# Kernel tuning notes

Hardware: AMD Instinct MI355X
Metric: run time of the kernel (lower is better)

## Reference

```python
import jax, jax.numpy as jnp
import numpy as np

N2, S2, M2 = 20000, 16000, 4000   # hop-2 frontier, hop-2 src fanout, hop-2 dst nodes
S1, M1 = 3500, 1024               # hop-1 src fanout, final batch
D_IN, D_H = 128, 128              # input_dim, internal_dim


def setup_inputs() -> dict:
    key = jax.random.key(0)
    ks = jax.random.split(key, 9)
    return {
        "src_nodes": jax.random.normal(ks[0], (N2, D_IN), dtype=jnp.float32),
        "dstsrc2src_1": jax.random.randint(ks[1], (S1,), 0, M2, dtype=jnp.int64),
        "dstsrc2src_2": jax.random.randint(ks[2], (S2,), 0, N2, dtype=jnp.int64),
        "dstsrc2dst_1": jax.random.randint(ks[3], (M1,), 0, M2, dtype=jnp.int64),
        "dstsrc2dst_2": jax.random.randint(ks[4], (M2,), 0, N2, dtype=jnp.int64),
        "dif_mat_1": jax.random.uniform(ks[5], (M1, S1), dtype=jnp.float32),
        "dif_mat_2": jax.random.uniform(ks[6], (M2, S2), dtype=jnp.float32),
        "w1": jax.random.normal(ks[7], (2 * D_IN, D_H), dtype=jnp.float32) * 0.06,
        "w2": jax.random.normal(ks[8], (2 * D_H, D_H), dtype=jnp.float32) * 0.06,
    }


def _mean_aggregate(feats, dstsrc2src, dstsrc2dst, dif_mat, w):
    # gather -> diffusion matmul -> concat -> linear -> relu
    dst_features = feats[dstsrc2dst]               # [M, d]
    src_features = feats[dstsrc2src]               # [S, d]
    aggregated = dif_mat @ src_features            # [M, d]
    concatenated = jnp.concatenate([aggregated, dst_features], axis=1)  # [M, 2d]
    return jax.nn.relu(concatenated @ w)           # [M, d_out]


def reference(src_nodes, dstsrc2src_1, dstsrc2src_2, dstsrc2dst_1,
              dstsrc2dst_2, dif_mat_1, dif_mat_2, w1, w2):
    # GraphSage.call: hop-2 aggregator first (with *_2 inputs), then hop-1.
    x = _mean_aggregate(src_nodes, dstsrc2src_2, dstsrc2dst_2, dif_mat_2, w1)
    x = _mean_aggregate(x, dstsrc2src_1, dstsrc2dst_1, dif_mat_1, w2)
    return x
```

## Files before the change

kernel.cpp:

```cpp
#include <hip/hip_runtime.h>

typedef __bf16 bf16x8 __attribute__((ext_vector_type(8)));
typedef float  f32x4  __attribute__((ext_vector_type(4)));
typedef unsigned short u16;
typedef u16 u16x8 __attribute__((ext_vector_type(8)));

__device__ __forceinline__ u16 f2bf(float f) {
    unsigned u = __builtin_bit_cast(unsigned, f);
    return (u16)((u + 0x7FFFu + ((u >> 16) & 1u)) >> 16);
}

__global__ __launch_bounds__(256) void gather_bt(
    const float* __restrict__ feats, const int* __restrict__ idx,
    u16* __restrict__ Bt, int Kcnt, int Kpad)
{
    __shared__ u16 st[128][66];
    const int tid = threadIdx.x;
    const int k0  = blockIdx.x * 64;

#pragma unroll
    for (int r2 = 0; r2 < 64; r2 += 2) {
        int r = r2 + (tid >> 7);
        int c = tid & 127;
        int k = k0 + r;
        float v = 0.f;
        if (k < Kcnt) v = feats[(size_t)idx[k] * 128 + c];
        st[c][r] = f2bf(v);
    }
    __syncthreads();

#pragma unroll
    for (int p = 0; p < 4; ++p) {
        int n  = p * 32 + (tid >> 3);
        int kk = (tid & 7) * 8;
        u16x8 v;
#pragma unroll
        for (int j = 0; j < 8; ++j) v[j] = st[n][kk + j];
        *(u16x8*)(Bt + (size_t)n * Kpad + k0 + kk) = v;
    }
}

__device__ __forceinline__ void loadA8(const float* __restrict__ ap, int koff,
                                       int K, f32x4& a0, f32x4& a1)
{
    if (koff + 8 <= K) {
        a0 = *(const f32x4*)(ap + koff);
        a1 = *(const f32x4*)(ap + koff + 4);
    } else {
#pragma unroll
        for (int j = 0; j < 4; ++j) {
            a0[j] = (koff + j     < K) ? ap[koff + j]     : 0.f;
            a1[j] = (koff + 4 + j < K) ? ap[koff + 4 + j] : 0.f;
        }
    }
}

__device__ __forceinline__ bf16x8 packA(f32x4 a0, f32x4 a1) {
    u16x8 h;
    h[0]=f2bf(a0[0]); h[1]=f2bf(a0[1]); h[2]=f2bf(a0[2]); h[3]=f2bf(a0[3]);
    h[4]=f2bf(a1[0]); h[5]=f2bf(a1[1]); h[6]=f2bf(a1[2]); h[7]=f2bf(a1[3]);
    return __builtin_bit_cast(bf16x8, h);
}

__global__ __launch_bounds__(256) void gemm_bt(
    const float* __restrict__ A, const u16* __restrict__ Bt,
    float* __restrict__ C, int M, int K, int Kpad, int sps)
{
    const int wid  = threadIdx.x >> 6;
    const int lane = threadIdx.x & 63;
    const int l15  = lane & 15;
    const int lhi  = lane >> 4;

    const int row0  = blockIdx.x * 64 + wid * 16;
    const int total = (K + 31) >> 5;
    int s0 = blockIdx.y * sps;
    int s1 = s0 + sps; if (s1 > total) s1 = total;
    if (s0 >= s1) return;

    f32x4 acc[8];
#pragma unroll
    for (int j = 0; j < 8; ++j) acc[j] = (f32x4){0.f, 0.f, 0.f, 0.f};

    const int rA = min(row0 + l15, M - 1);
    const float* __restrict__ ap = A + (size_t)rA * K;
    const u16*   __restrict__ btl = Bt + (size_t)l15 * Kpad + lhi * 8;

    f32x4 ra0, ra1;
    loadA8(ap, (s0 << 5) + lhi * 8, K, ra0, ra1);

    for (int s = s0; s < s1; ++s) {
        const int k0 = s << 5;

        f32x4 na0, na1;
        if (s + 1 < s1) loadA8(ap, ((s + 1) << 5) + lhi * 8, K, na0, na1);

        bf16x8 bfr[8];
#pragma unroll
        for (int cf = 0; cf < 8; ++cf)
            bfr[cf] = __builtin_bit_cast(bf16x8,
                *(const u16x8*)(btl + (size_t)cf * 16 * Kpad + k0));

        bf16x8 af = packA(ra0, ra1);
#pragma unroll
        for (int cf = 0; cf < 8; ++cf)
            acc[cf] = __builtin_amdgcn_mfma_f32_16x16x32_bf16(af, bfr[cf], acc[cf], 0, 0, 0);

        ra0 = na0; ra1 = na1;
    }

#pragma unroll
    for (int cf = 0; cf < 8; ++cf)
#pragma unroll
        for (int i = 0; i < 4; ++i) {
            int r = row0 + lhi * 4 + i;
            if (r < M)
                atomicAdd(C + (size_t)r * 128 + cf * 16 + l15, acc[cf][i]);
        }
}

__global__ __launch_bounds__(256) void dense_relu(
    const float* __restrict__ agg, const float* __restrict__ fsrc,
    const int* __restrict__ didx, const float* __restrict__ w,
    float* __restrict__ out, int M)
{
    __shared__ float sb[32][257];
    const int tid  = threadIdx.x;
    const int row0 = blockIdx.x * 32;

    for (int i = tid; i < 32 * 32; i += 256) {
        int r = i >> 5, c4 = (i & 31) << 2;
        int gr = row0 + r;
        f32x4 v = (f32x4){0.f, 0.f, 0.f, 0.f};
        if (gr < M) v = *(const f32x4*)(agg + (size_t)gr * 128 + c4);
        sb[r][c4 + 0] = v[0]; sb[r][c4 + 1] = v[1];
        sb[r][c4 + 2] = v[2]; sb[r][c4 + 3] = v[3];
    }
    for (int i = tid; i < 32 * 32; i += 256) {
        int r = i >> 5, c4 = (i & 31) << 2;
        int gr = row0 + r;
        int sr = (gr < M) ? didx[gr] : 0;
        f32x4 v = *(const f32x4*)(fsrc + (size_t)sr * 128 + c4);
        sb[r][128 + c4 + 0] = v[0]; sb[r][128 + c4 + 1] = v[1];
        sb[r][128 + c4 + 2] = v[2]; sb[r][128 + c4 + 3] = v[3];
    }
    __syncthreads();

    const int colg = (tid & 15) << 3;
    const int r0l  = (tid >> 4) * 2;
    float acc0[8], acc1[8];
#pragma unroll
    for (int c = 0; c < 8; ++c) { acc0[c] = 0.f; acc1[c] = 0.f; }

    for (int j = 0; j < 256; ++j) {
        f32x4 wa = *(const f32x4*)(w + j * 128 + colg);
        f32x4 wb = *(const f32x4*)(w + j * 128 + colg + 4);
        float a0 = sb[r0l][j];
        float a1 = sb[r0l + 1][j];
#pragma unroll
        for (int c = 0; c < 4; ++c) {
            acc0[c]     += a0 * wa[c];  acc0[c + 4] += a0 * wb[c];
            acc1[c]     += a1 * wa[c];  acc1[c + 4] += a1 * wb[c];
        }
    }

    int gr0 = row0 + r0l;
    if (gr0 < M) {
#pragma unroll
        for (int c = 0; c < 8; ++c)
            out[(size_t)gr0 * 128 + colg + c] = fmaxf(acc0[c], 0.f);
    }
    int gr1 = gr0 + 1;
    if (gr1 < M) {
#pragma unroll
        for (int c = 0; c < 8; ++c)
            out[(size_t)gr1 * 128 + colg + c] = fmaxf(acc1[c], 0.f);
    }
}

extern "C" void kernel_launch(void* const* d_in, const int* in_sizes, int n_in,
                              void* d_out, int out_size, void* d_ws, size_t ws_size,
                              hipStream_t stream)
{
    const float* src_nodes = (const float*)d_in[0];
    const int*   s1idx     = (const int*)d_in[1];
    const int*   s2idx     = (const int*)d_in[2];
    const int*   d1idx     = (const int*)d_in[3];
    const int*   d2idx     = (const int*)d_in[4];
    const float* dif1      = (const float*)d_in[5];
    const float* dif2      = (const float*)d_in[6];
    const float* w1        = (const float*)d_in[7];
    const float* w2        = (const float*)d_in[8];
    float*       out       = (float*)d_out;

    const int S2 = 16000, M2 = 4000, S1 = 3500, M1 = 1024;
    const int K2 = 16000, K1 = 3500;
    const int Kpad2 = 16000;
    const int Kpad1 = 3520;

    char* ws = (char*)d_ws;
    size_t off = 0;
    float* agg2 = (float*)(ws + off); off += (size_t)M2 * 128 * 4;
    float* agg1 = (float*)(ws + off); off += (size_t)M1 * 128 * 4;
    float* x    = (float*)(ws + off); off += (size_t)M2 * 128 * 4;
    u16*   Bt2  = (u16*)(ws + off);   off += (size_t)128 * Kpad2 * 2;
    u16*   Bt1  = (u16*)(ws + off);   off += (size_t)128 * Kpad1 * 2;

    hipMemsetAsync(agg2, 0, (size_t)(M2 + M1) * 128 * 4, stream);

    gather_bt<<<Kpad2 / 64, 256, 0, stream>>>(src_nodes, s2idx, Bt2, S2, Kpad2);

    {
        dim3 grid((M2 + 63) / 64, 10);
        gemm_bt<<<grid, 256, 0, stream>>>(dif2, Bt2, agg2, M2, K2, Kpad2, 50);
    }

    dense_relu<<<(M2 + 31) / 32, 256, 0, stream>>>(agg2, src_nodes, d2idx, w1, x, M2);

    gather_bt<<<Kpad1 / 64, 256, 0, stream>>>(x, s1idx, Bt1, S1, Kpad1);

    {
        dim3 grid((M1 + 63) / 64, 22);
        gemm_bt<<<grid, 256, 0, stream>>>(dif1, Bt1, agg1, M1, K1, Kpad1, 5);
    }

    dense_relu<<<(M1 + 31) / 32, 256, 0, stream>>>(agg1, x, d1idx, w2, out, M1);
}
```

Measured before the change: 579.0 us.

## Batch A loads per 256-wide K chunk and double-buffer B fragments in GEMM

The split-K GEMM now works in 256-wide K chunks, issuing all sixteen A vector loads for a chunk at once and prefetching the next step's B fragments into registers while the current MFMAs run. Kpad is enlarged and the workspace padded so the B prefetch past the end stays in bounds, and the split-K grid and spans are retuned to the new chunk size. The aim is to raise memory-level parallelism and hide global load latency in this bandwidth-bound kernel. The cost is higher register pressure, with launch_bounds set to 2 blocks per SM, plus a 4x unroll of the dense_relu inner loop.

```diff
diff --git a/kernel.cpp b/kernel.cpp
--- a/kernel.cpp
+++ b/kernel.cpp
@@ -8,6 +8,13 @@
 __device__ __forceinline__ u16 f2bf(float f) {
     unsigned u = __builtin_bit_cast(unsigned, f);
     return (u16)((u + 0x7FFFu + ((u >> 16) & 1u)) >> 16);
+}
+
+__device__ __forceinline__ bf16x8 packA(f32x4 a0, f32x4 a1) {
+    u16x8 h;
+    h[0]=f2bf(a0[0]); h[1]=f2bf(a0[1]); h[2]=f2bf(a0[2]); h[3]=f2bf(a0[3]);
+    h[4]=f2bf(a1[0]); h[5]=f2bf(a1[1]); h[6]=f2bf(a1[2]); h[7]=f2bf(a1[3]);
+    return __builtin_bit_cast(bf16x8, h);
 }
 
 __global__ __launch_bounds__(256) void gather_bt(
@@ -40,72 +47,80 @@
     }
 }
 
-__device__ __forceinline__ void loadA8(const float* __restrict__ ap, int koff,
-                                       int K, f32x4& a0, f32x4& a1)
-{
-    if (koff + 8 <= K) {
-        a0 = *(const f32x4*)(ap + koff);
-        a1 = *(const f32x4*)(ap + koff + 4);
-    } else {
-#pragma unroll
-        for (int j = 0; j < 4; ++j) {
-            a0[j] = (koff + j     < K) ? ap[koff + j]     : 0.f;
-            a1[j] = (koff + 4 + j < K) ? ap[koff + 4 + j] : 0.f;
-        }
-    }
-}
-
-__device__ __forceinline__ bf16x8 packA(f32x4 a0, f32x4 a1) {
-    u16x8 h;
-    h[0]=f2bf(a0[0]); h[1]=f2bf(a0[1]); h[2]=f2bf(a0[2]); h[3]=f2bf(a0[3]);
-    h[4]=f2bf(a1[0]); h[5]=f2bf(a1[1]); h[6]=f2bf(a1[2]); h[7]=f2bf(a1[3]);
-    return __builtin_bit_cast(bf16x8, h);
-}
-
-__global__ __launch_bounds__(256) void gemm_bt(
+__global__ __launch_bounds__(256, 2) void gemm_bt(
     const float* __restrict__ A, const u16* __restrict__ Bt,
-    float* __restrict__ C, int M, int K, int Kpad, int sps)
+    float* __restrict__ C, int M, int K, int Kpad, int mspan)
 {
     const int wid  = threadIdx.x >> 6;
     const int lane = threadIdx.x & 63;
     const int l15  = lane & 15;
     const int lhi  = lane >> 4;
 
-    const int row0  = blockIdx.x * 64 + wid * 16;
-    const int total = (K + 31) >> 5;
-    int s0 = blockIdx.y * sps;
-    int s1 = s0 + sps; if (s1 > total) s1 = total;
-    if (s0 >= s1) return;
+    const int row0 = blockIdx.x * 64 + wid * 16;
+    const int macro_total = (K + 255) >> 8;
+    int m0 = blockIdx.y * mspan;
+    int m1 = m0 + mspan; if (m1 > macro_total) m1 = macro_total;
+    if (m0 >= m1) return;
 
     f32x4 acc[8];
 #pragma unroll
     for (int j = 0; j < 8; ++j) acc[j] = (f32x4){0.f, 0.f, 0.f, 0.f};
 
     const int rA = min(row0 + l15, M - 1);
-    const float* __restrict__ ap = A + (size_t)rA * K;
+    const float* __restrict__ ap  = A + (size_t)rA * K;
     const u16*   __restrict__ btl = Bt + (size_t)l15 * Kpad + lhi * 8;
 
-    f32x4 ra0, ra1;
-    loadA8(ap, (s0 << 5) + lhi * 8, K, ra0, ra1);
-
-    for (int s = s0; s < s1; ++s) {
-        const int k0 = s << 5;
-
-        f32x4 na0, na1;
-        if (s + 1 < s1) loadA8(ap, ((s + 1) << 5) + lhi * 8, K, na0, na1);
-
-        bf16x8 bfr[8];
+    bf16x8 bcur[8];
+    {
+        const int kf = m0 << 8;
 #pragma unroll
         for (int cf = 0; cf < 8; ++cf)
-            bfr[cf] = __builtin_bit_cast(bf16x8,
-                *(const u16x8*)(btl + (size_t)cf * 16 * Kpad + k0));
-
-        bf16x8 af = packA(ra0, ra1);
-#pragma unroll
-        for (int cf = 0; cf < 8; ++cf)
-            acc[cf] = __builtin_amdgcn_mfma_f32_16x16x32_bf16(af, bfr[cf], acc[cf], 0, 0, 0);
-
-        ra0 = na0; ra1 = na1;
+            bcur[cf] = __builtin_bit_cast(bf16x8,
+                *(const u16x8*)(btl + (size_t)cf * 16 * Kpad + kf));
+    }
+
+    for (int m = m0; m < m1; ++m) {
+        const int kbase = m << 8;
+
+        f32x4 araw[16];
+        if (kbase + 256 <= K) {
+#pragma unroll
+            for (int j = 0; j < 8; ++j) {
+                const int koff = kbase + j * 32 + lhi * 8;
+                araw[2 * j]     = *(const f32x4*)(ap + koff);
+                araw[2 * j + 1] = *(const f32x4*)(ap + koff + 4);
+            }
+        } else {
+#pragma unroll
+            for (int j = 0; j < 8; ++j) {
+                const int koff = kbase + j * 32 + lhi * 8;
+                f32x4 a0, a1;
+#pragma unroll
+                for (int e = 0; e < 4; ++e) {
+                    a0[e] = (koff + e     < K) ? ap[koff + e]     : 0.f;
+                    a1[e] = (koff + 4 + e < K) ? ap[koff + 4 + e] : 0.f;
+                }
+                araw[2 * j] = a0; araw[2 * j + 1] = a1;
+            }
+        }
+
+#pragma unroll
+        for (int j = 0; j < 8; ++j) {
+            const int knext = kbase + j * 32 + 32;
+            bf16x8 bnxt[8];
+#pragma unroll
+            for (int cf = 0; cf < 8; ++cf)
+                bnxt[cf] = __builtin_bit_cast(bf16x8,
+                    *(const u16x8*)(btl + (size_t)cf * 16 * Kpad + knext));
+
+            const bf16x8 af = packA(araw[2 * j], araw[2 * j + 1]);
+#pragma unroll
+            for (int cf = 0; cf < 8; ++cf)
+                acc[cf] = __builtin_amdgcn_mfma_f32_16x16x32_bf16(af, bcur[cf], acc[cf], 0, 0, 0);
+
+#pragma unroll
+            for (int cf = 0; cf < 8; ++cf) bcur[cf] = bnxt[cf];
+        }
     }
 
 #pragma unroll
@@ -151,6 +166,7 @@
 #pragma unroll
     for (int c = 0; c < 8; ++c) { acc0[c] = 0.f; acc1[c] = 0.f; }
 
+#pragma unroll 4
     for (int j = 0; j < 256; ++j) {
         f32x4 wa = *(const f32x4*)(w + j * 128 + colg);
         f32x4 wb = *(const f32x4*)(w + j * 128 + colg + 4);
@@ -194,24 +210,24 @@
 
     const int S2 = 16000, M2 = 4000, S1 = 3500, M1 = 1024;
     const int K2 = 16000, K1 = 3500;
-    const int Kpad2 = 16000;
-    const int Kpad1 = 3520;
+    const int Kpad2 = 16128;
+    const int Kpad1 = 3584;
 
     char* ws = (char*)d_ws;
     size_t off = 0;
     float* agg2 = (float*)(ws + off); off += (size_t)M2 * 128 * 4;
     float* agg1 = (float*)(ws + off); off += (size_t)M1 * 128 * 4;
     float* x    = (float*)(ws + off); off += (size_t)M2 * 128 * 4;
-    u16*   Bt2  = (u16*)(ws + off);   off += (size_t)128 * Kpad2 * 2;
-    u16*   Bt1  = (u16*)(ws + off);   off += (size_t)128 * Kpad1 * 2;
+    u16*   Bt2  = (u16*)(ws + off);   off += (size_t)128 * Kpad2 * 2 + 512;
+    u16*   Bt1  = (u16*)(ws + off);   off += (size_t)128 * Kpad1 * 2 + 512;
 
     hipMemsetAsync(agg2, 0, (size_t)(M2 + M1) * 128 * 4, stream);
 
     gather_bt<<<Kpad2 / 64, 256, 0, stream>>>(src_nodes, s2idx, Bt2, S2, Kpad2);
 
     {
-        dim3 grid((M2 + 63) / 64, 10);
-        gemm_bt<<<grid, 256, 0, stream>>>(dif2, Bt2, agg2, M2, K2, Kpad2, 50);
+        dim3 grid((M2 + 63) / 64, 8);
+        gemm_bt<<<grid, 256, 0, stream>>>(dif2, Bt2, agg2, M2, K2, Kpad2, 8);
     }
 
     dense_relu<<<(M2 + 31) / 32, 256, 0, stream>>>(agg2, src_nodes, d2idx, w1, x, M2);
@@ -219,8 +235,8 @@
     gather_bt<<<Kpad1 / 64, 256, 0, stream>>>(x, s1idx, Bt1, S1, Kpad1);
 
     {
-        dim3 grid((M1 + 63) / 64, 22);
-        gemm_bt<<<grid, 256, 0, stream>>>(dif1, Bt1, agg1, M1, K1, Kpad1, 5);
+        dim3 grid((M1 + 63) / 64, 14);
+        gemm_bt<<<grid, 256, 0, stream>>>(dif1, Bt1, agg1, M1, K1, Kpad1, 1);
     }
 
     dense_relu<<<(M1 + 31) / 32, 256, 0, stream>>>(agg1, x, d1idx, w2, out, M1);
```

Result: no change. 588.1 us (+1.6%).
